# Kernel optimization log

Hardware: AMD Instinct MI355X
Metric: run time of the kernel (lower is better)

Reference implementation:

```python
import jax, jax.numpy as jnp
import numpy as np

B, S, R, D_NODE, D_PAIR, N_HEAD, C = 1, 128, 256, 256, 128, 8, 32
EPS = 1e-5


def layer_norm(x, g, b):
    mu = jnp.mean(x, axis=-1, keepdims=True)
    var = jnp.mean(jnp.square(x - mu), axis=-1, keepdims=True)
    return (x - mu) * jax.lax.rsqrt(var + EPS) * g + b


def self_attention(x, qkv_w, qkv_b, gate_w, gate_b, o_w, o_b, bias=None):
    # x: [B, n1, n2, d]; attends over n2. heads: n_head x c, n_head*c == d.
    b_, n1, n2, d = x.shape
    qkv = x @ qkv_w.T + qkv_b                      # [B, n1, n2, 3*h*c]
    q, k, v = jnp.split(qkv, 3, axis=-1)
    split_heads = lambda t: t.reshape(b_, n1, n2, N_HEAD, C).transpose(0, 1, 3, 2, 4)  # [B,n1,h,n2,c]
    q = split_heads(q) * (C ** -0.5)
    k = split_heads(k)
    v = split_heads(v)
    logits = jnp.einsum('bshqc,bshkc->bshqk', q, k)  # [B, n1, h, n2, n2]
    if bias is not None:
        logits = logits + bias[:, None]              # bias: [B, h, n2, n2]
    w = jax.nn.softmax(logits, axis=-1)
    o = jnp.einsum('bshqk,bshkc->bshqc', w, v)
    o = o.transpose(0, 1, 3, 2, 4).reshape(b_, n1, n2, N_HEAD * C)
    gate = jax.nn.sigmoid(x @ gate_w.T + gate_b)
    o = o * gate
    out = o @ o_w.T
    if o_b is not None:
        out = out + o_b
    return out


def setup_inputs() -> dict:
    key = jax.random.key(0)
    ks = jax.random.split(key, 12)
    rn = lambda k, sh, sc=1.0: jax.random.normal(k, sh, dtype=jnp.float32) * sc
    return {
        'node': rn(ks[0], (B, S, R, D_NODE)),
        'pair': rn(ks[1], (B, R, R, D_PAIR)),
        'ln_mr_g': jnp.ones((D_NODE,), jnp.float32), 'ln_mr_b': jnp.zeros((D_NODE,), jnp.float32),
        'ln_z_g': jnp.ones((D_PAIR,), jnp.float32), 'ln_z_b': jnp.zeros((D_PAIR,), jnp.float32),
        'b_weights': rn(ks[2], (N_HEAD, D_PAIR), D_PAIR ** -0.5),
        'row_qkv_w': rn(ks[3], (3 * N_HEAD * C, D_NODE), D_NODE ** -0.5),
        'row_qkv_b': jnp.zeros((3 * N_HEAD * C,), jnp.float32),
        'row_gate_w': rn(ks[4], (N_HEAD * C, D_NODE), D_NODE ** -0.5),
        'row_gate_b': jnp.ones((N_HEAD * C,), jnp.float32),
        'row_o_w': rn(ks[5], (D_NODE, N_HEAD * C), D_NODE ** -0.5),
        'out_bias': jnp.zeros((D_NODE,), jnp.float32),
        'ln_mc_g': jnp.ones((D_NODE,), jnp.float32), 'ln_mc_b': jnp.zeros((D_NODE,), jnp.float32),
        'col_qkv_w': rn(ks[6], (3 * N_HEAD * C, D_NODE), D_NODE ** -0.5),
        'col_qkv_b': jnp.zeros((3 * N_HEAD * C,), jnp.float32),
        'col_gate_w': rn(ks[7], (N_HEAD * C, D_NODE), D_NODE ** -0.5),
        'col_gate_b': jnp.ones((N_HEAD * C,), jnp.float32),
        'col_o_w': rn(ks[8], (D_NODE, N_HEAD * C), D_NODE ** -0.5),
        'col_o_b': jnp.zeros((D_NODE,), jnp.float32),
        'ln_t_g': jnp.ones((D_NODE,), jnp.float32), 'ln_t_b': jnp.zeros((D_NODE,), jnp.float32),
        't_w1': rn(ks[9], (4 * D_NODE, D_NODE), D_NODE ** -0.5),
        't_b1': jnp.zeros((4 * D_NODE,), jnp.float32),
        't_w2': rn(ks[10], (D_NODE, 4 * D_NODE), (4 * D_NODE) ** -0.5),
        't_b2': jnp.zeros((D_NODE,), jnp.float32),
    }


def reference(node, pair, ln_mr_g, ln_mr_b, ln_z_g, ln_z_b, b_weights,
              row_qkv_w, row_qkv_b, row_gate_w, row_gate_b, row_o_w, out_bias,
              ln_mc_g, ln_mc_b, col_qkv_w, col_qkv_b, col_gate_w, col_gate_b, col_o_w, col_o_b,
              ln_t_g, ln_t_b, t_w1, t_b1, t_w2, t_b2):
    # --- MSARowAttentionWithPairBias ---
    M = layer_norm(node, ln_mr_g, ln_mr_b)                 # [B,S,R,D]
    Z = layer_norm(pair, ln_z_g, ln_z_b)                   # [B,R,R,Dp]
    b = jnp.einsum('bqkd,hd->bhqk', Z, b_weights)          # pair bias [B,h,R,R]
    M = self_attention(M, row_qkv_w, row_qkv_b, row_gate_w, row_gate_b, row_o_w, None, bias=b)
    # bias_dropout_add with ones dropout mask (inference): residual + (x + bias)
    node = node + M + out_bias
    # --- MSAColumnAttention ---
    Mt = node.transpose(0, 2, 1, 3)                        # [B,R,S,D], attend over S
    Mt = layer_norm(Mt, ln_mc_g, ln_mc_b)
    Mt = self_attention(Mt, col_qkv_w, col_qkv_b, col_gate_w, col_gate_b, col_o_w, col_o_b)
    node = node + Mt.transpose(0, 2, 1, 3)
    # --- MSATransition (n=4) ---
    x = layer_norm(node, ln_t_g, ln_t_b)
    x = jax.nn.relu(x @ t_w1.T + t_b1) @ t_w2.T + t_b2
    return node + x
```

## Files before the change

kernel.cpp:

```cpp
#include <hip/hip_runtime.h>
#include <hip/hip_bf16.h>

#define EPS 1e-5f

typedef __hip_bfloat16 bf16;
typedef __attribute__((ext_vector_type(8))) short short8v;
typedef __attribute__((ext_vector_type(4))) short short4v;
typedef __attribute__((ext_vector_type(4))) float f32x4;

__device__ inline f32x4 mfma16bf(short4v a, short4v b, f32x4 c) {
#if __has_builtin(__builtin_amdgcn_mfma_f32_16x16x16bf16_1k)
  return __builtin_amdgcn_mfma_f32_16x16x16bf16_1k(a, b, c, 0, 0, 0);
#else
  short8v a8 = {a[0], a[1], a[2], a[3], 0, 0, 0, 0};
  short8v b8 = {b[0], b[1], b[2], b[3], 0, 0, 0, 0};
  return __builtin_amdgcn_mfma_f32_16x16x32_bf16(a8, b8, c, 0, 0, 0);
#endif
}

__device__ inline void load_lds16(const void* g, void* l) {
  __builtin_amdgcn_global_load_lds(
      (const __attribute__((address_space(1))) void*)g,
      (__attribute__((address_space(3))) void*)l, 16, 0, 0);
}

__device__ inline unsigned pack_bf16x2(float a, float b) {
  union { bf16 h[2]; unsigned u; } cv;
  cv.h[0] = __float2bfloat16(a);
  cv.h[1] = __float2bfloat16(b);
  return cv.u;
}

__device__ inline float4 bf4_to_f4(ushort4 u) {
  union { ushort4 u4; bf16 h[4]; } c;
  c.u4 = u;
  return make_float4(__bfloat162float(c.h[0]), __bfloat162float(c.h[1]),
                     __bfloat162float(c.h[2]), __bfloat162float(c.h[3]));
}

#define L2E 1.4426950408889634f
#define QSCALE_L2E 0.25504333961883236f

struct CvtArgs {
  const float* src[8];
  bf16* dst[8];
  int n4[8];
  int scale_n4[8];
};

__global__ __launch_bounds__(256) void cvt_all_kernel(CvtArgs a) {
  int i = blockIdx.x * 256 + threadIdx.x;
#pragma unroll
  for (int s = 0; s < 8; ++s) {
    if (i < a.n4[s]) {
      float4 v = reinterpret_cast<const float4*>(a.src[s])[i];
      float sc = (i < a.scale_n4[s]) ? QSCALE_L2E : 1.0f;
      union { ushort4 u; bf16 h[4]; } cv;
      cv.h[0] = __float2bfloat16(v.x * sc);
      cv.h[1] = __float2bfloat16(v.y * sc);
      cv.h[2] = __float2bfloat16(v.z * sc);
      cv.h[3] = __float2bfloat16(v.w * sc);
      reinterpret_cast<ushort4*>(a.dst[s])[i] = cv.u;
      return;
    }
    i -= a.n4[s];
  }
}

__global__ __launch_bounds__(256) void bias_concat_kernel(
    const float* rq, const float* rg, const float* cq, const float* cg,
    float* br, float* bc) {
  int i = blockIdx.x * 256 + threadIdx.x;
  if (i < 1024) {
    float v = (i < 768) ? rq[i] : rg[i - 768];
    br[i] = (i < 256) ? v * QSCALE_L2E : v;
  } else {
    int j = i - 1024;
    float v = (j < 768) ? cq[j] : cg[j - 768];
    bc[j] = (j < 256) ? v * QSCALE_L2E : v;
  }
}

template <int INB>
__global__ __launch_bounds__(512) void ln256_bf_kernel(
    const void* __restrict__ in, bf16* __restrict__ out,
    const float* __restrict__ g, const float* __restrict__ b) {
  int tid = threadIdx.x;
  int w = tid >> 6, lane = tid & 63;
  int row0 = blockIdx.x * 16 + w * 2;
  float4 x0, x1;
  if (INB) {
    const bf16* inB = (const bf16*)in;
    x0 = bf4_to_f4(
        reinterpret_cast<const ushort4*>(inB + (size_t)row0 * 256)[lane]);
    x1 = bf4_to_f4(
        reinterpret_cast<const ushort4*>(inB + (size_t)(row0 + 1) * 256)[lane]);
  } else {
    const float* inF = (const float*)in;
    x0 = reinterpret_cast<const float4*>(inF + (size_t)row0 * 256)[lane];
    x1 = reinterpret_cast<const float4*>(inF + (size_t)(row0 + 1) * 256)[lane];
  }
  float4 gv = reinterpret_cast<const float4*>(g)[lane];
  float4 bv = reinterpret_cast<const float4*>(b)[lane];

  float s0 = x0.x + x0.y + x0.z + x0.w;
  float q0 = x0.x * x0.x + x0.y * x0.y + x0.z * x0.z + x0.w * x0.w;
  float s1 = x1.x + x1.y + x1.z + x1.w;
  float q1 = x1.x * x1.x + x1.y * x1.y + x1.z * x1.z + x1.w * x1.w;
#pragma unroll
  for (int off = 32; off >= 1; off >>= 1) {
    s0 += __shfl_xor(s0, off);
    q0 += __shfl_xor(q0, off);
    s1 += __shfl_xor(s1, off);
    q1 += __shfl_xor(q1, off);
  }
  float m0 = s0 * (1.0f / 256.0f);
  float i0 = rsqrtf(q0 * (1.0f / 256.0f) - m0 * m0 + EPS);
  float m1 = s1 * (1.0f / 256.0f);
  float i1 = rsqrtf(q1 * (1.0f / 256.0f) - m1 * m1 + EPS);

  union { ushort4 u; bf16 h[4]; } c0, c1;
  c0.h[0] = __float2bfloat16((x0.x - m0) * i0 * gv.x + bv.x);
  c0.h[1] = __float2bfloat16((x0.y - m0) * i0 * gv.y + bv.y);
  c0.h[2] = __float2bfloat16((x0.z - m0) * i0 * gv.z + bv.z);
  c0.h[3] = __float2bfloat16((x0.w - m0) * i0 * gv.w + bv.w);
  c1.h[0] = __float2bfloat16((x1.x - m1) * i1 * gv.x + bv.x);
  c1.h[1] = __float2bfloat16((x1.y - m1) * i1 * gv.y + bv.y);
  c1.h[2] = __float2bfloat16((x1.z - m1) * i1 * gv.z + bv.z);
  c1.h[3] = __float2bfloat16((x1.w - m1) * i1 * gv.w + bv.w);
  reinterpret_cast<ushort4*>(out + (size_t)row0 * 256)[lane] = c0.u;
  reinterpret_cast<ushort4*>(out + (size_t)(row0 + 1) * 256)[lane] = c1.u;
}

__global__ __launch_bounds__(256) void pair_bias_kernel(
    const float* __restrict__ pair, const float* __restrict__ g,
    const float* __restrict__ b, const float* __restrict__ bw,
    float* __restrict__ bT) {
  int tid = threadIdx.x;
  int w = tid >> 6, lane = tid & 63;
  int l15 = lane & 15, l4 = lane >> 4;
  int rowbase = blockIdx.x * 64 + w * 16;
  const float* zrow = pair + (size_t)(rowbase + l15) * 128;

  float z[4][8];
#pragma unroll
  for (int kk = 0; kk < 4; ++kk) {
    float4 a0 = *reinterpret_cast<const float4*>(zrow + kk * 32 + l4 * 8);
    float4 a1 = *reinterpret_cast<const float4*>(zrow + kk * 32 + l4 * 8 + 4);
    z[kk][0] = a0.x; z[kk][1] = a0.y; z[kk][2] = a0.z; z[kk][3] = a0.w;
    z[kk][4] = a1.x; z[kk][5] = a1.y; z[kk][6] = a1.z; z[kk][7] = a1.w;
  }
  float s = 0.0f, sq = 0.0f;
#pragma unroll
  for (int kk = 0; kk < 4; ++kk)
#pragma unroll
    for (int e = 0; e < 8; ++e) {
      s += z[kk][e];
      sq += z[kk][e] * z[kk][e];
    }
  s += __shfl_xor(s, 16);
  s += __shfl_xor(s, 32);
  sq += __shfl_xor(sq, 16);
  sq += __shfl_xor(sq, 32);
  float mu = s * (1.0f / 128.0f);
  float inv = rsqrtf(sq * (1.0f / 128.0f) - mu * mu + EPS);

  f32x4 acc = {0.f, 0.f, 0.f, 0.f};
#pragma unroll
  for (int kk = 0; kk < 4; ++kk) {
    const float* gp = g + kk * 32 + l4 * 8;
    const float* bp = b + kk * 32 + l4 * 8;
    float4 g0 = *reinterpret_cast<const float4*>(gp);
    float4 g1 = *reinterpret_cast<const float4*>(gp + 4);
    float4 b0 = *reinterpret_cast<const float4*>(bp);
    float4 b1 = *reinterpret_cast<const float4*>(bp + 4);
    float gv[8] = {g0.x, g0.y, g0.z, g0.w, g1.x, g1.y, g1.z, g1.w};
    float bv[8] = {b0.x, b0.y, b0.z, b0.w, b1.x, b1.y, b1.z, b1.w};
    union { short8v v; bf16 h[8]; } af;
#pragma unroll
    for (int e = 0; e < 8; ++e)
      af.h[e] = __float2bfloat16((z[kk][e] - mu) * inv * gv[e] + bv[e]);
    union { short8v v; bf16 h[8]; } bwf;
    if (l15 < 8) {
      const float* wp = bw + l15 * 128 + kk * 32 + l4 * 8;
      float4 w0 = *reinterpret_cast<const float4*>(wp);
      float4 w1 = *reinterpret_cast<const float4*>(wp + 4);
      float wv[8] = {w0.x, w0.y, w0.z, w0.w, w1.x, w1.y, w1.z, w1.w};
#pragma unroll
      for (int e = 0; e < 8; ++e) bwf.h[e] = __float2bfloat16(wv[e]);
    } else {
      bwf.v = short8v{0, 0, 0, 0, 0, 0, 0, 0};
    }
    acc = __builtin_amdgcn_mfma_f32_16x16x32_bf16(af.v, bwf.v, acc, 0, 0, 0);
  }
  if (l15 < 8) {
    float4 o4 =
        make_float4(acc[0] * L2E, acc[1] * L2E, acc[2] * L2E, acc[3] * L2E);
    *reinterpret_cast<float4*>(&bT[(size_t)l15 * 65536 + rowbase + l4 * 4]) =
        o4;
  }
}

template <int EPI, int AMAP, int OMAP, int AUXB, int OUTB>
__global__ __launch_bounds__(256) void gemm_mfma_kernel(
    const bf16* __restrict__ A, const bf16* __restrict__ W,
    const float* __restrict__ bias, const void* __restrict__ aux, void* out,
    int N, int K, int nbn) {
  __shared__ __align__(16) short As[2][128 * 32];
  __shared__ __align__(16) short Bs[2][128 * 32];
  int nwg = gridDim.x;
  int qch = nwg >> 3;
  int flat = blockIdx.x;
  int wg = (flat & 7) * qch + (flat >> 3);
  int bm = wg / nbn, bn = wg % nbn;
  int tid = threadIdx.x;
  int w = tid >> 6, lane = tid & 63;
  int wr = w >> 1, wc = w & 1;
  int c0 = w * 64 + lane;
  int srow = c0 >> 2, skq = c0 & 3;
  const short* Aptr = (const short*)A;
  const short* Wbase = (const short*)(W + (size_t)(bn * 128) * K);
  f32x4 acc[4][4] = {};
  int lrow = lane & 15, kq = lane >> 4;

  auto arow = [&](int r) -> size_t {
    return AMAP ? ((size_t)r * 256 + bm) : ((size_t)(bm * 128 + r));
  };
  auto stage = [&](int buf, int k0) {
    load_lds16(Aptr + arow(srow) * K + k0 + skq * 8, &As[buf][c0 * 8]);
    load_lds16(Aptr + arow(srow + 64) * K + k0 + skq * 8,
               &As[buf][(256 + c0) * 8]);
    load_lds16(Wbase + (size_t)srow * K + k0 + skq * 8, &Bs[buf][c0 * 8]);
    load_lds16(Wbase + (size_t)(srow + 64) * K + k0 + skq * 8,
               &Bs[buf][(256 + c0) * 8]);
  };

  stage(0, 0);
  __syncthreads();
  int nk = K >> 5;
  for (int t = 0; t < nk; ++t) {
    int cur = t & 1;
    if (t + 1 < nk) stage(cur ^ 1, (t + 1) << 5);
    short8v af[4], bfv[4];
#pragma unroll
    for (int i = 0; i < 4; ++i)
      af[i] = *reinterpret_cast<const short8v*>(
          &As[cur][(wr * 64 + i * 16 + lrow) * 32 + kq * 8]);
#pragma unroll
    for (int j = 0; j < 4; ++j)
      bfv[j] = *reinterpret_cast<const short8v*>(
          &Bs[cur][(wc * 64 + j * 16 + lrow) * 32 + kq * 8]);
#pragma unroll
    for (int i = 0; i < 4; ++i)
#pragma unroll
      for (int j = 0; j < 4; ++j)
        acc[i][j] = __builtin_amdgcn_mfma_f32_16x16x32_bf16(bfv[j], af[i],
                                                            acc[i][j], 0, 0, 0);
    __syncthreads();
  }

  float* outF = (float*)out;
  bf16* outB = (bf16*)out;
  const float* auxF = (const float*)aux;
  const bf16* auxB = (const bf16*)aux;
#pragma unroll
  for (int j = 0; j < 4; ++j) {
    int cc = bn * 128 + wc * 64 + j * 16 + kq * 4;
    float4 bv4 = bias ? *reinterpret_cast<const float4*>(bias + cc)
                      : make_float4(0.f, 0.f, 0.f, 0.f);
#pragma unroll
    for (int i = 0; i < 4; ++i) {
      int lr = wr * 64 + i * 16 + lrow;
      size_t off = OMAP ? (((size_t)lr * 256 + bm) * N + cc)
                        : ((size_t)(bm * 128 + lr) * N + cc);
      float v0 = acc[i][j][0] + bv4.x;
      float v1 = acc[i][j][1] + bv4.y;
      float v2 = acc[i][j][2] + bv4.z;
      float v3 = acc[i][j][3] + bv4.w;
      if (EPI == 2) {
        float4 av = AUXB
                        ? bf4_to_f4(*reinterpret_cast<const ushort4*>(auxB + off))
                        : *reinterpret_cast<const float4*>(auxF + off);
        v0 += av.x; v1 += av.y; v2 += av.z; v3 += av.w;
      } else if (EPI == 3) {
        v0 = fmaxf(v0, 0.0f); v1 = fmaxf(v1, 0.0f);
        v2 = fmaxf(v2, 0.0f); v3 = fmaxf(v3, 0.0f);
      }
      if (OUTB || EPI == 0 || EPI == 3) {
        union { ushort4 u; bf16 h[4]; } cv;
        cv.h[0] = __float2bfloat16(v0);
        cv.h[1] = __float2bfloat16(v1);
        cv.h[2] = __float2bfloat16(v2);
        cv.h[3] = __float2bfloat16(v3);
        *reinterpret_cast<ushort4*>(outB + off) = cv.u;
      } else {
        *reinterpret_cast<float4*>(outF + off) = make_float4(v0, v1, v2, v3);
      }
    }
  }
}

template <bool ROWMODE>
__global__ __launch_bounds__(512) void attn_mfma_kernel(
    const bf16* __restrict__ qkv, const float* __restrict__ bT,
    bf16* __restrict__ o) {
  constexpr int KVLEN = ROWMODE ? 256 : 128;
  constexpr int NSUB = ROWMODE ? 1 : 2;
  constexpr int QT = 2;
  constexpr int KOUT = KVLEN / 64;
  constexpr int KSZ = KVLEN * 32;
  __shared__ __align__(16) short K_lds[NSUB * KSZ];
  __shared__ __align__(16) short Vt_lds[NSUB * 32 * KVLEN];

  int b = blockIdx.x;
  int idx = b >> 3, h = b & 7;
  int tid = threadIdx.x;
  int w = tid >> 6, lane = tid & 63;
  int l15 = lane & 15, l4 = lane >> 4;
  int sub = ROWMODE ? 0 : (w >> 2);
  const short* qb =
      (const short*)qkv + ((size_t)idx * NSUB + sub) * (KVLEN * 1024);
  const bf16* qbh = (const bf16*)qb;
  bf16* ob = o + ((size_t)idx * NSUB + sub) * (KVLEN * 256);

#pragma unroll
  for (int rnd = 0; rnd < 2; ++rnd) {
    int c = rnd * 512 + tid;
    int sc = c / (KVLEN * 4);
    int cc = c - sc * (KVLEN * 4);
    int row = cc >> 2;
    int kq = (cc & 3) ^ ((row >> 1) & 3);
    const short* qs =
        (const short*)qkv + ((size_t)idx * NSUB + sc) * (KVLEN * 1024);
    load_lds16(qs + (size_t)row * 1024 + 256 + h * 32 + kq * 8,
               &K_lds[sc * KSZ + cc * 8]);
  }
  {
    int tt = tid;
    int sv = tt / (KVLEN * 2);
    int t2 = tt - sv * (KVLEN * 2);
    int kp = t2 >> 2;
    int cc = (t2 & 3) * 8;
    const short* qs =
        (const short*)qkv + ((size_t)idx * NSUB + sv) * (KVLEN * 1024);
    short8v va = *reinterpret_cast<const short8v*>(
        qs + (size_t)(2 * kp) * 1024 + 512 + h * 32 + cc);
    short8v vb = *reinterpret_cast<const short8v*>(
        qs + (size_t)(2 * kp + 1) * 1024 + 512 + h * 32 + cc);
    int k = 2 * kp;
    int u = k >> 3;
    int klo = k & 7;
#pragma unroll
    for (int e = 0; e < 8; ++e) {
      int cI = cc + e;
      int up = u ^ (cI & 7);
      unsigned pk = (unsigned)(unsigned short)va[e] |
                    ((unsigned)(unsigned short)vb[e] << 16);
      *reinterpret_cast<unsigned*>(
          &Vt_lds[sv * 32 * KVLEN + cI * KVLEN + up * 8 + klo]) = pk;
    }
  }
  __syncthreads();

  int q0 = (ROWMODE ? w : (w & 3)) * 32;
  short8v qf[QT];
#pragma unroll
  for (int j = 0; j < QT; ++j)
    qf[j] = *reinterpret_cast<const short8v*>(
        qb + (size_t)(q0 + j * 16 + l15) * 1024 + h * 32 + l4 * 8);

  f32x4 acc_o[QT][2] = {};
  f32x4 acc_l[QT] = {};
  const short4v ones = {0x3F80, 0x3F80, 0x3F80, 0x3F80};
  const f32x4 zf = {0.f, 0.f, 0.f, 0.f};

  f32x4 accs[4];
  short4v P[4];
  float4 bb[4];
  const short* Kb = &K_lds[sub * KSZ];
  const short* Vb = &Vt_lds[sub * 32 * KVLEN];

#define LOAD_BIAS(KT, JJ)                                                   \
  if (ROWMODE) {                                                            \
    const float* bq_ = bT + (size_t)h * 65536 +                             \
                       (size_t)(q0 + (JJ) * 16 + l15) * 256 + (KT) * 64 +   \
                       l4 * 4;                                              \
    _Pragma("unroll") for (int i_ = 0; i_ < 4; ++i_) bb[i_] =               \
        *reinterpret_cast<const float4*>(bq_ + i_ * 16);                    \
  }

#define DO_QK(KT, JJ)                                                       \
  {                                                                         \
    _Pragma("unroll") for (int i_ = 0; i_ < 4; ++i_) {                      \
      int krow_ = (KT) * 64 + i_ * 16 + l15;                                \
      short8v kf_ = *reinterpret_cast<const short8v*>(                      \
          &Kb[krow_ * 32 + ((l4 ^ ((krow_ >> 1) & 3)) * 8)]);               \
      f32x4 cin_ = zf;                                                      \
      if (ROWMODE) {                                                        \
        cin_[0] = bb[i_].x; cin_[1] = bb[i_].y;                             \
        cin_[2] = bb[i_].z; cin_[3] = bb[i_].w;                             \
      }                                                                     \
      accs[i_] = __builtin_amdgcn_mfma_f32_16x16x32_bf16(kf_, qf[JJ], cin_, \
                                                         0, 0, 0);          \
    }                                                                       \
  }

#define DO_EXPPACK()                                                        \
  {                                                                         \
    _Pragma("unroll") for (int i_ = 0; i_ < 4; ++i_) {                      \
      float t0_ = exp2f(accs[i_][0]);                                       \
      float t1_ = exp2f(accs[i_][1]);                                       \
      float t2_ = exp2f(accs[i_][2]);                                       \
      float t3_ = exp2f(accs[i_][3]);                                       \
      union { unsigned u2[2]; short4v s; } pb_;                             \
      pb_.u2[0] = pack_bf16x2(t0_, t1_);                                    \
      pb_.u2[1] = pack_bf16x2(t2_, t3_);                                    \
      P[i_] = pb_.s;                                                        \
    }                                                                       \
  }

#define DO_PV(KT, JJ)                                                       \
  {                                                                         \
    _Pragma("unroll") for (int ks_ = 0; ks_ < 4; ++ks_) {                   \
      _Pragma("unroll") for (int ct_ = 0; ct_ < 2; ++ct_) {                 \
        int cI_ = ct_ * 16 + l15;                                           \
        int u_ = (KT) * 8 + ks_ * 2 + (l4 >> 1);                            \
        short4v vf_ = *reinterpret_cast<const short4v*>(                    \
            &Vb[cI_ * KVLEN + (u_ ^ (cI_ & 7)) * 8 + (l4 & 1) * 4]);        \
        acc_o[JJ][ct_] = mfma16bf(vf_, P[ks_], acc_o[JJ][ct_]);             \
      }                                                                     \
      acc_l[JJ] = mfma16bf(ones, P[ks_], acc_l[JJ]);                        \
    }                                                                       \
  }

  LOAD_BIAS(0, 0);
  DO_QK(0, 0);
  LOAD_BIAS(0, 1);
  DO_EXPPACK();
#pragma unroll 1
  for (int kt = 0; kt < KOUT; ++kt) {
    DO_QK(kt, 1);
    if (kt + 1 < KOUT) LOAD_BIAS(kt + 1, 0);
    DO_PV(kt, 0);
    DO_EXPPACK();
    if (kt + 1 < KOUT) {
      DO_QK(kt + 1, 0);
      LOAD_BIAS(kt + 1, 1);
      DO_PV(kt, 1);
      DO_EXPPACK();
    }
  }
  DO_PV(KOUT - 1, 1);
#undef LOAD_BIAS
#undef DO_QK
#undef DO_EXPPACK
#undef DO_PV

#pragma unroll
  for (int j = 0; j < QT; ++j) {
    float inv = 1.0f / acc_l[j][0];
    int row = q0 + j * 16 + l15;
    const bf16* grow = qbh + (size_t)row * 1024 + 768 + h * 32;
    bf16* orow = ob + (size_t)row * 256 + h * 32;
#pragma unroll
    for (int ct = 0; ct < 2; ++ct) {
      int cc = ct * 16 + l4 * 4;
      ushort4 gv = *reinterpret_cast<const ushort4*>(grow + cc);
      union { ushort4 u; bf16 h4[4]; } gu, ou;
      gu.u = gv;
#pragma unroll
      for (int r = 0; r < 4; ++r) {
        float gt = __bfloat162float(gu.h4[r]);
        float sg = 1.0f / (1.0f + __expf(-gt));
        ou.h4[r] = __float2bfloat16(acc_o[j][ct][r] * inv * sg);
      }
      *reinterpret_cast<ushort4*>(orow + cc) = ou.u;
    }
  }
}

extern "C" void kernel_launch(void* const* d_in, const int* in_sizes, int n_in,
                              void* d_out, int out_size, void* d_ws,
                              size_t ws_size, hipStream_t stream) {
  (void)in_sizes; (void)n_in; (void)out_size; (void)ws_size;
  const float* node      = (const float*)d_in[0];
  const float* pair      = (const float*)d_in[1];
  const float* ln_mr_g   = (const float*)d_in[2];
  const float* ln_mr_b   = (const float*)d_in[3];
  const float* ln_z_g    = (const float*)d_in[4];
  const float* ln_z_b    = (const float*)d_in[5];
  const float* b_weights = (const float*)d_in[6];
  const float* row_qkv_w = (const float*)d_in[7];
  const float* row_qkv_b = (const float*)d_in[8];
  const float* row_gate_w= (const float*)d_in[9];
  const float* row_gate_b= (const float*)d_in[10];
  const float* row_o_w   = (const float*)d_in[11];
  const float* out_bias  = (const float*)d_in[12];
  const float* ln_mc_g   = (const float*)d_in[13];
  const float* ln_mc_b   = (const float*)d_in[14];
  const float* col_qkv_w = (const float*)d_in[15];
  const float* col_qkv_b = (const float*)d_in[16];
  const float* col_gate_w= (const float*)d_in[17];
  const float* col_gate_b= (const float*)d_in[18];
  const float* col_o_w   = (const float*)d_in[19];
  const float* col_o_b   = (const float*)d_in[20];
  const float* ln_t_g    = (const float*)d_in[21];
  const float* ln_t_b    = (const float*)d_in[22];
  const float* t_w1      = (const float*)d_in[23];
  const float* t_b1      = (const float*)d_in[24];
  const float* t_w2      = (const float*)d_in[25];
  const float* t_b2      = (const float*)d_in[26];
  float* out = (float*)d_out;

  const size_t NR = 32768;
  char* p = (char*)d_ws;
  bf16* nodeB     = (bf16*)p;  p += NR * 256 * 2;
  char*  qkv_region = p;       p += NR * 1024 * 2;
  float* buf_bias = (float*)p; p += 8 * 256 * 256 * 4;
  bf16* ln_bf     = (bf16*)p;  p += NR * 256 * 2;
  bf16* g_bf      = (bf16*)p;  p += NR * 256 * 2;
  bf16* qkv_bf = (bf16*)qkv_region;
  bf16* h_bf   = (bf16*)qkv_region;
  bf16* w_rqkvg = (bf16*)p; p += 1024 * 256 * 2;
  bf16* w_ro    = (bf16*)p; p += 256 * 256 * 2;
  bf16* w_cqkvg = (bf16*)p; p += 1024 * 256 * 2;
  bf16* w_co    = (bf16*)p; p += 256 * 256 * 2;
  bf16* w_t1    = (bf16*)p; p += 1024 * 256 * 2;
  bf16* w_t2    = (bf16*)p; p += 256 * 1024 * 2;
  float* b_rqkvg = (float*)p; p += 1024 * 4;
  float* b_cqkvg = (float*)p; p += 1024 * 4;

  CvtArgs ca;
  ca.src[0] = row_qkv_w;  ca.dst[0] = w_rqkvg;             ca.n4[0] = 49152;
  ca.src[1] = row_gate_w; ca.dst[1] = w_rqkvg + 768 * 256; ca.n4[1] = 16384;
  ca.src[2] = row_o_w;    ca.dst[2] = w_ro;                ca.n4[2] = 16384;
  ca.src[3] = col_qkv_w;  ca.dst[3] = w_cqkvg;             ca.n4[3] = 49152;
  ca.src[4] = col_gate_w; ca.dst[4] = w_cqkvg + 768 * 256; ca.n4[4] = 16384;
  ca.src[5] = col_o_w;    ca.dst[5] = w_co;                ca.n4[5] = 16384;
  ca.src[6] = t_w1;       ca.dst[6] = w_t1;                ca.n4[6] = 65536;
  ca.src[7] = t_w2;       ca.dst[7] = w_t2;                ca.n4[7] = 65536;
  for (int s = 0; s < 8; ++s) ca.scale_n4[s] = 0;
  ca.scale_n4[0] = 16384;
  ca.scale_n4[3] = 16384;
  cvt_all_kernel<<<1152, 256, 0, stream>>>(ca);
  bias_concat_kernel<<<8, 256, 0, stream>>>(row_qkv_b, row_gate_b, col_qkv_b,
                                            col_gate_b, b_rqkvg, b_cqkvg);

  ln256_bf_kernel<0><<<2048, 512, 0, stream>>>(node, ln_bf, ln_mr_g, ln_mr_b);
  pair_bias_kernel<<<1024, 256, 0, stream>>>(pair, ln_z_g, ln_z_b, b_weights,
                                             buf_bias);
  gemm_mfma_kernel<0, 0, 0, 0, 0><<<2048, 256, 0, stream>>>(
      ln_bf, w_rqkvg, b_rqkvg, nullptr, qkv_bf, 1024, 256, 8);
  attn_mfma_kernel<true><<<1024, 512, 0, stream>>>(qkv_bf, buf_bias, g_bf);
  gemm_mfma_kernel<2, 0, 0, 0, 1><<<512, 256, 0, stream>>>(
      g_bf, w_ro, out_bias, node, nodeB, 256, 256, 2);

  ln256_bf_kernel<1><<<2048, 512, 0, stream>>>(nodeB, ln_bf, ln_mc_g, ln_mc_b);
  gemm_mfma_kernel<0, 1, 0, 0, 0><<<2048, 256, 0, stream>>>(
      ln_bf, w_cqkvg, b_cqkvg, nullptr, qkv_bf, 1024, 256, 8);
  attn_mfma_kernel<false><<<1024, 512, 0, stream>>>(qkv_bf, nullptr, g_bf);
  gemm_mfma_kernel<2, 0, 1, 1, 1><<<512, 256, 0, stream>>>(
      g_bf, w_co, col_o_b, nodeB, nodeB, 256, 256, 2);

  ln256_bf_kernel<1><<<2048, 512, 0, stream>>>(nodeB, ln_bf, ln_t_g, ln_t_b);
  gemm_mfma_kernel<3, 0, 0, 0, 0><<<2048, 256, 0, stream>>>(
      ln_bf, w_t1, t_b1, nullptr, h_bf, 1024, 256, 8);
  gemm_mfma_kernel<2, 0, 0, 1, 0><<<512, 256, 0, stream>>>(
      h_bf, w_t2, t_b2, nodeB, out, 256, 1024, 2);
}
```

Before: 292.6 us.

## Fold column and transition LayerNorms into GEMM epilogues via precomputed stats

The column-attention and transition LayerNorms are no longer written out as normalized bf16 activations. A small stats kernel computes per-row mean*inv and inv, the gamma scale is folded into the bf16 weights, and beta is folded into a precomputed bias. The GEMM epilogue then applies inv*acc - mean*inv*c1 + beta, so the GEMMs read the raw bf16 residual directly and one normalized-activation write and read per LayerNorm is avoided. The cost is an extra prep kernel and a stats pass that still reads the full rows. Numerics change slightly because the mean is subtracted after the bf16 matmul.

```diff
diff --git a/kernel.cpp b/kernel.cpp
--- a/kernel.cpp
+++ b/kernel.cpp
@@ -44,6 +44,7 @@
 struct CvtArgs {
   const float* src[8];
   bf16* dst[8];
+  const float* gvec[8];
   int n4[8];
   int scale_n4[8];
 };
@@ -55,11 +56,14 @@
     if (i < a.n4[s]) {
       float4 v = reinterpret_cast<const float4*>(a.src[s])[i];
       float sc = (i < a.scale_n4[s]) ? QSCALE_L2E : 1.0f;
+      float4 gv = make_float4(1.f, 1.f, 1.f, 1.f);
+      if (a.gvec[s])
+        gv = *reinterpret_cast<const float4*>(a.gvec[s] + (i & 63) * 4);
       union { ushort4 u; bf16 h[4]; } cv;
-      cv.h[0] = __float2bfloat16(v.x * sc);
-      cv.h[1] = __float2bfloat16(v.y * sc);
-      cv.h[2] = __float2bfloat16(v.z * sc);
-      cv.h[3] = __float2bfloat16(v.w * sc);
+      cv.h[0] = __float2bfloat16(v.x * sc * gv.x);
+      cv.h[1] = __float2bfloat16(v.y * sc * gv.y);
+      cv.h[2] = __float2bfloat16(v.z * sc * gv.z);
+      cv.h[3] = __float2bfloat16(v.w * sc * gv.w);
       reinterpret_cast<ushort4*>(a.dst[s])[i] = cv.u;
       return;
     }
@@ -68,38 +72,95 @@
 }
 
 __global__ __launch_bounds__(256) void bias_concat_kernel(
-    const float* rq, const float* rg, const float* cq, const float* cg,
-    float* br, float* bc) {
+    const float* rq, const float* rg, float* br) {
   int i = blockIdx.x * 256 + threadIdx.x;
-  if (i < 1024) {
-    float v = (i < 768) ? rq[i] : rg[i - 768];
-    br[i] = (i < 256) ? v * QSCALE_L2E : v;
+  float v = (i < 768) ? rq[i] : rg[i - 768];
+  br[i] = (i < 256) ? v * QSCALE_L2E : v;
+}
+
+__global__ __launch_bounds__(256) void lnfuse_prep_kernel(
+    const float* cqkv_w, const float* cgate_w, const float* cqkv_b,
+    const float* cgate_b, const float* mc_g, const float* mc_b,
+    const float* t1_w, const float* t1_b, const float* t_g, const float* t_b_,
+    float* c1c, float* betac, float* c1t, float* betat) {
+  int wid = blockIdx.x * 4 + (threadIdx.x >> 6);
+  int lane = threadIdx.x & 63;
+  bool isT = wid >= 1024;
+  int n = isT ? wid - 1024 : wid;
+  const float* Wrow;
+  float bias0;
+  const float *g, *bb;
+  if (isT) {
+    Wrow = t1_w + (size_t)n * 256; bias0 = t1_b[n]; g = t_g; bb = t_b_;
+  } else if (n < 768) {
+    Wrow = cqkv_w + (size_t)n * 256; bias0 = cqkv_b[n]; g = mc_g; bb = mc_b;
   } else {
-    int j = i - 1024;
-    float v = (j < 768) ? cq[j] : cg[j - 768];
-    bc[j] = (j < 256) ? v * QSCALE_L2E : v;
-  }
-}
-
-template <int INB>
+    Wrow = cgate_w + (size_t)(n - 768) * 256; bias0 = cgate_b[n - 768];
+    g = mc_g; bb = mc_b;
+  }
+  float4 wv = *reinterpret_cast<const float4*>(Wrow + lane * 4);
+  float4 gv = *reinterpret_cast<const float4*>(g + lane * 4);
+  float4 bv = *reinterpret_cast<const float4*>(bb + lane * 4);
+  float s1 = wv.x * gv.x + wv.y * gv.y + wv.z * gv.z + wv.w * gv.w;
+  float s2 = wv.x * bv.x + wv.y * bv.y + wv.z * bv.z + wv.w * bv.w;
+#pragma unroll
+  for (int off = 32; off >= 1; off >>= 1) {
+    s1 += __shfl_xor(s1, off);
+    s2 += __shfl_xor(s2, off);
+  }
+  if (lane == 0) {
+    float s = (!isT && n < 256) ? QSCALE_L2E : 1.0f;
+    if (isT) {
+      c1t[n] = s1;
+      betat[n] = bias0 + s2;
+    } else {
+      c1c[n] = s * s1;
+      betac[n] = s * (bias0 + s2);
+    }
+  }
+}
+
+__global__ __launch_bounds__(512) void ln_stats_kernel(
+    const bf16* __restrict__ in, float2* __restrict__ st) {
+  int tid = threadIdx.x;
+  int w = tid >> 6, lane = tid & 63;
+  int row0 = blockIdx.x * 16 + w * 2;
+  float4 x0 = bf4_to_f4(
+      reinterpret_cast<const ushort4*>(in + (size_t)row0 * 256)[lane]);
+  float4 x1 = bf4_to_f4(
+      reinterpret_cast<const ushort4*>(in + (size_t)(row0 + 1) * 256)[lane]);
+  float s0 = x0.x + x0.y + x0.z + x0.w;
+  float q0 = x0.x * x0.x + x0.y * x0.y + x0.z * x0.z + x0.w * x0.w;
+  float s1 = x1.x + x1.y + x1.z + x1.w;
+  float q1 = x1.x * x1.x + x1.y * x1.y + x1.z * x1.z + x1.w * x1.w;
+#pragma unroll
+  for (int off = 32; off >= 1; off >>= 1) {
+    s0 += __shfl_xor(s0, off);
+    q0 += __shfl_xor(q0, off);
+    s1 += __shfl_xor(s1, off);
+    q1 += __shfl_xor(q1, off);
+  }
+  if (lane == 0) {
+    float m0 = s0 * (1.0f / 256.0f);
+    float i0 = rsqrtf(q0 * (1.0f / 256.0f) - m0 * m0 + EPS);
+    st[row0] = make_float2(m0 * i0, i0);
+  }
+  if (lane == 32) {
+    float m1 = s1 * (1.0f / 256.0f);
+    float i1 = rsqrtf(q1 * (1.0f / 256.0f) - m1 * m1 + EPS);
+    st[row0 + 1] = make_float2(m1 * i1, i1);
+  }
+}
+
 __global__ __launch_bounds__(512) void ln256_bf_kernel(
-    const void* __restrict__ in, bf16* __restrict__ out,
+    const float* __restrict__ in, bf16* __restrict__ out,
     const float* __restrict__ g, const float* __restrict__ b) {
   int tid = threadIdx.x;
   int w = tid >> 6, lane = tid & 63;
   int row0 = blockIdx.x * 16 + w * 2;
-  float4 x0, x1;
-  if (INB) {
-    const bf16* inB = (const bf16*)in;
-    x0 = bf4_to_f4(
-        reinterpret_cast<const ushort4*>(inB + (size_t)row0 * 256)[lane]);
-    x1 = bf4_to_f4(
-        reinterpret_cast<const ushort4*>(inB + (size_t)(row0 + 1) * 256)[lane]);
-  } else {
-    const float* inF = (const float*)in;
-    x0 = reinterpret_cast<const float4*>(inF + (size_t)row0 * 256)[lane];
-    x1 = reinterpret_cast<const float4*>(inF + (size_t)(row0 + 1) * 256)[lane];
-  }
+  float4 x0 = reinterpret_cast<const float4*>(in + (size_t)row0 * 256)[lane];
+  float4 x1 =
+      reinterpret_cast<const float4*>(in + (size_t)(row0 + 1) * 256)[lane];
   float4 gv = reinterpret_cast<const float4*>(g)[lane];
   float4 bv = reinterpret_cast<const float4*>(b)[lane];
 
@@ -201,11 +262,12 @@
   }
 }
 
-template <int EPI, int AMAP, int OMAP, int AUXB, int OUTB>
+template <int EPI, int AMAP, int OMAP, int AUXB, int OUTB, int LNF>
 __global__ __launch_bounds__(256) void gemm_mfma_kernel(
     const bf16* __restrict__ A, const bf16* __restrict__ W,
     const float* __restrict__ bias, const void* __restrict__ aux, void* out,
-    int N, int K, int nbn) {
+    int N, int K, int nbn, const float2* __restrict__ stats,
+    const float* __restrict__ c1) {
   __shared__ __align__(16) short As[2][128 * 32];
   __shared__ __align__(16) short Bs[2][128 * 32];
   int nwg = gridDim.x;
@@ -259,6 +321,13 @@
     __syncthreads();
   }
 
+  float2 stv[4];
+  if (LNF) {
+#pragma unroll
+    for (int i = 0; i < 4; ++i)
+      stv[i] = stats[arow(wr * 64 + i * 16 + lrow)];
+  }
+
   float* outF = (float*)out;
   bf16* outB = (bf16*)out;
   const float* auxF = (const float*)aux;
@@ -268,15 +337,26 @@
     int cc = bn * 128 + wc * 64 + j * 16 + kq * 4;
     float4 bv4 = bias ? *reinterpret_cast<const float4*>(bias + cc)
                       : make_float4(0.f, 0.f, 0.f, 0.f);
+    float4 c1v = make_float4(0.f, 0.f, 0.f, 0.f);
+    if (LNF) c1v = *reinterpret_cast<const float4*>(c1 + cc);
 #pragma unroll
     for (int i = 0; i < 4; ++i) {
       int lr = wr * 64 + i * 16 + lrow;
       size_t off = OMAP ? (((size_t)lr * 256 + bm) * N + cc)
                         : ((size_t)(bm * 128 + lr) * N + cc);
-      float v0 = acc[i][j][0] + bv4.x;
-      float v1 = acc[i][j][1] + bv4.y;
-      float v2 = acc[i][j][2] + bv4.z;
-      float v3 = acc[i][j][3] + bv4.w;
+      float v0, v1, v2, v3;
+      if (LNF) {
+        float inv = stv[i].y, mi = stv[i].x;
+        v0 = inv * acc[i][j][0] - mi * c1v.x + bv4.x;
+        v1 = inv * acc[i][j][1] - mi * c1v.y + bv4.y;
+        v2 = inv * acc[i][j][2] - mi * c1v.z + bv4.z;
+        v3 = inv * acc[i][j][3] - mi * c1v.w + bv4.w;
+      } else {
+        v0 = acc[i][j][0] + bv4.x;
+        v1 = acc[i][j][1] + bv4.y;
+        v2 = acc[i][j][2] + bv4.z;
+        v3 = acc[i][j][3] + bv4.w;
+      }
       if (EPI == 2) {
         float4 av = AUXB
                         ? bf4_to_f4(*reinterpret_cast<const ushort4*>(auxB + off))
@@ -528,7 +608,11 @@
   bf16* w_t1    = (bf16*)p; p += 1024 * 256 * 2;
   bf16* w_t2    = (bf16*)p; p += 256 * 1024 * 2;
   float* b_rqkvg = (float*)p; p += 1024 * 4;
-  float* b_cqkvg = (float*)p; p += 1024 * 4;
+  float* c1c    = (float*)p; p += 1024 * 4;
+  float* betac  = (float*)p; p += 1024 * 4;
+  float* c1t    = (float*)p; p += 1024 * 4;
+  float* betat  = (float*)p; p += 1024 * 4;
+  float2* lstats = (float2*)p; p += NR * 8;
 
   CvtArgs ca;
   ca.src[0] = row_qkv_w;  ca.dst[0] = w_rqkvg;             ca.n4[0] = 49152;
@@ -539,32 +623,38 @@
   ca.src[5] = col_o_w;    ca.dst[5] = w_co;                ca.n4[5] = 16384;
   ca.src[6] = t_w1;       ca.dst[6] = w_t1;                ca.n4[6] = 65536;
   ca.src[7] = t_w2;       ca.dst[7] = w_t2;                ca.n4[7] = 65536;
-  for (int s = 0; s < 8; ++s) ca.scale_n4[s] = 0;
+  for (int s = 0; s < 8; ++s) { ca.scale_n4[s] = 0; ca.gvec[s] = nullptr; }
   ca.scale_n4[0] = 16384;
   ca.scale_n4[3] = 16384;
+  ca.gvec[3] = ln_mc_g;
+  ca.gvec[4] = ln_mc_g;
+  ca.gvec[6] = ln_t_g;
   cvt_all_kernel<<<1152, 256, 0, stream>>>(ca);
-  bias_concat_kernel<<<8, 256, 0, stream>>>(row_qkv_b, row_gate_b, col_qkv_b,
-                                            col_gate_b, b_rqkvg, b_cqkvg);
-
-  ln256_bf_kernel<0><<<2048, 512, 0, stream>>>(node, ln_bf, ln_mr_g, ln_mr_b);
+  bias_concat_kernel<<<4, 256, 0, stream>>>(row_qkv_b, row_gate_b, b_rqkvg);
+  lnfuse_prep_kernel<<<512, 256, 0, stream>>>(
+      col_qkv_w, col_gate_w, col_qkv_b, col_gate_b, ln_mc_g, ln_mc_b, t_w1,
+      t_b1, ln_t_g, ln_t_b, c1c, betac, c1t, betat);
+
+  ln256_bf_kernel<<<2048, 512, 0, stream>>>(node, ln_bf, ln_mr_g, ln_mr_b);
   pair_bias_kernel<<<1024, 256, 0, stream>>>(pair, ln_z_g, ln_z_b, b_weights,
                                              buf_bias);
-  gemm_mfma_kernel<0, 0, 0, 0, 0><<<2048, 256, 0, stream>>>(
-      ln_bf, w_rqkvg, b_rqkvg, nullptr, qkv_bf, 1024, 256, 8);
+  gemm_mfma_kernel<0, 0, 0, 0, 0, 0><<<2048, 256, 0, stream>>>(
+      ln_bf, w_rqkvg, b_rqkvg, nullptr, qkv_bf, 1024, 256, 8, nullptr,
+      nullptr);
   attn_mfma_kernel<true><<<1024, 512, 0, stream>>>(qkv_bf, buf_bias, g_bf);
-  gemm_mfma_kernel<2, 0, 0, 0, 1><<<512, 256, 0, stream>>>(
-      g_bf, w_ro, out_bias, node, nodeB, 256, 256, 2);
-
-  ln256_bf_kernel<1><<<2048, 512, 0, stream>>>(nodeB, ln_bf, ln_mc_g, ln_mc_b);
-  gemm_mfma_kernel<0, 1, 0, 0, 0><<<2048, 256, 0, stream>>>(
-      ln_bf, w_cqkvg, b_cqkvg, nullptr, qkv_bf, 1024, 256, 8);
+  gemm_mfma_kernel<2, 0, 0, 0, 1, 0><<<512, 256, 0, stream>>>(
+      g_bf, w_ro, out_bias, node, nodeB, 256, 256, 2, nullptr, nullptr);
+
+  ln_stats_kernel<<<2048, 512, 0, stream>>>(nodeB, lstats);
+  gemm_mfma_kernel<0, 1, 0, 0, 0, 1><<<2048, 256, 0, stream>>>(
+      nodeB, w_cqkvg, betac, nullptr, qkv_bf, 1024, 256, 8, lstats, c1c);
   attn_mfma_kernel<false><<<1024, 512, 0, stream>>>(qkv_bf, nullptr, g_bf);
-  gemm_mfma_kernel<2, 0, 1, 1, 1><<<512, 256, 0, stream>>>(
-      g_bf, w_co, col_o_b, nodeB, nodeB, 256, 256, 2);
-
-  ln256_bf_kernel<1><<<2048, 512, 0, stream>>>(nodeB, ln_bf, ln_t_g, ln_t_b);
-  gemm_mfma_kernel<3, 0, 0, 0, 0><<<2048, 256, 0, stream>>>(
-      ln_bf, w_t1, t_b1, nullptr, h_bf, 1024, 256, 8);
-  gemm_mfma_kernel<2, 0, 0, 1, 0><<<512, 256, 0, stream>>>(
-      h_bf, w_t2, t_b2, nodeB, out, 256, 1024, 2);
-}
+  gemm_mfma_kernel<2, 0, 1, 1, 1, 0><<<512, 256, 0, stream>>>(
+      g_bf, w_co, col_o_b, nodeB, nodeB, 256, 256, 2, nullptr, nullptr);
+
+  ln_stats_kernel<<<2048, 512, 0, stream>>>(nodeB, lstats);
+  gemm_mfma_kernel<3, 0, 0, 0, 0, 1><<<2048, 256, 0, stream>>>(
+      nodeB, w_t1, betat, nullptr, h_bf, 1024, 256, 8, lstats, c1t);
+  gemm_mfma_kernel<2, 0, 0, 1, 0, 0><<<512, 256, 0, stream>>>(
+      h_bf, w_t2, t_b2, nodeB, out, 256, 1024, 2, nullptr, nullptr);
+}
```

New measurement: 306.6 us. 1.05x slower.
